# Kernel optimization log

Measured on AMD Instinct MI355X. Metric: run time of the kernel, lower is better.

## Reference

```python
import jax, jax.numpy as jnp
import numpy as np

B, N, D_IN, D_OUT = 8, 2048, 64, 64
ALPHA = 0.2          # LeakyReLU negative slope
MASK_FILL = -9e15    # matches -9000000000000000.0 in the torch code
P_EDGE = 0.05


def _build_adj(key):
    # base random adjacency [N,N], then block structure [[adj, I],[0, adj]]
    base = (jax.random.uniform(key, (N, N)) < P_EDGE).astype(jnp.float32)
    eye = jnp.eye(N, dtype=jnp.float32)
    top = jnp.concatenate([base, eye], axis=1)
    bot = jnp.concatenate([jnp.zeros((N, N), jnp.float32), base], axis=1)
    return jnp.concatenate([top, bot], axis=0)  # [2N, 2N]


def setup_inputs() -> dict:
    key = jax.random.key(0)
    k1, k2, k3, k4, k5, k6 = jax.random.split(key, 6)
    h = jax.random.normal(k1, (B, N, D_IN), jnp.float32)
    ht = jax.random.normal(k2, (B, N, D_IN), jnp.float32)
    # xavier_uniform-ish scale for params
    W = jax.random.normal(k3, (D_IN, D_OUT), jnp.float32) * 0.15
    a1 = jax.random.normal(k4, (D_OUT, 1), jnp.float32) * 0.15
    a2 = jax.random.normal(k5, (D_OUT, 1), jnp.float32) * 0.15
    adj = _build_adj(k6)
    return {"h": h, "ht": ht, "W": W, "a1": a1, "a2": a2, "adj": adj}


def reference(h, ht, W, a1, a2, adj):
    # concat along node dim: [b, 2n, d_in]
    hc = jnp.concatenate([ht, h], axis=1)
    Wh = jnp.einsum('bni,io->bno', hc, W)           # [b, 2n, d_out]
    # additive attention scores: Wh1_i + Wh2_j, LeakyReLU
    Wh1 = Wh @ a1                                    # [b, 2n, 1]
    Wh2 = Wh @ a2                                    # [b, 2n, 1]
    e = Wh1 + jnp.swapaxes(Wh2, 1, 2)                # [b, 2n, 2n]
    e = jnp.where(e > 0, e, ALPHA * e)               # LeakyReLU
    att = jnp.where(adj > 0, e, MASK_FILL)
    att = jax.nn.softmax(att, axis=1)                # NOTE: dim=1 as in torch code
    # dropout is identity in eval mode
    hp = jnp.matmul(att, Wh)                         # [b, 2n, d_out]
    n = adj.shape[0] // 2
    hp = jnp.concatenate([hp[:, :n], hp[:, n:]], axis=-1)  # [b, n, 2*d_out]
    return jax.nn.elu(hp)                            # concat=True -> ELU
```

## Files before the change

### kernel.cpp

```cpp
#include <hip/hip_runtime.h>
#include <hip/hip_bf16.h>
#include <math.h>

#define BB 8
#define NN 2048
#define TN 4096
#define DD 64

typedef __attribute__((ext_vector_type(8))) short short8;
typedef __attribute__((ext_vector_type(4))) float f32x4;
typedef __attribute__((ext_vector_type(4))) unsigned int u32x4;

__device__ __forceinline__ unsigned short f2bf(float f) {
    union { float f; unsigned int i; } v; v.f = f;
    unsigned int r = v.i + 0x7FFF + ((v.i >> 16) & 1);
    return (unsigned short)(r >> 16);
}
__device__ __forceinline__ float bf2f(unsigned short u) {
    union { unsigned int i; float f; } v; v.i = ((unsigned int)u) << 16; return v.f;
}

__global__ __launch_bounds__(256, 4) void k1_wh(
                      const float* __restrict__ h,
                      const float* __restrict__ ht,
                      const float* __restrict__ W,
                      const float* __restrict__ a1,
                      const float* __restrict__ a2,
                      float* __restrict__ Wh,
                      float* __restrict__ E1p, float* __restrict__ E1n,
                      float* __restrict__ E2p, float* __restrict__ E2n,
                      float* __restrict__ E1i) {
    __shared__ float xs[4][512];
    int tid = threadIdx.x;
    int w = tid >> 6, l = tid & 63;
    float wreg[64];
    #pragma unroll
    for (int k = 0; k < 64; ++k) wreg[k] = W[k * 64 + l];
    float a1l = a1[l], a2l = a2[l];
    int rowbase = (blockIdx.x * 4 + w) * 8;
    int b = rowbase >> 12;
    int m0 = rowbase & (TN - 1);
    const float* srcw = (m0 < NN) ? (ht + ((size_t)b * NN + m0) * DD)
                                  : (h  + ((size_t)b * NN + (m0 - NN)) * DD);
    f32x4 g0 = *reinterpret_cast<const f32x4*>(srcw + l * 8);
    f32x4 g1 = *reinterpret_cast<const f32x4*>(srcw + l * 8 + 4);
    *reinterpret_cast<f32x4*>(&xs[w][l * 8])     = g0;
    *reinterpret_cast<f32x4*>(&xs[w][l * 8 + 4]) = g1;
    __syncthreads();
    for (int r = 0; r < 8; ++r) {
        const f32x4* xr = reinterpret_cast<const f32x4*>(&xs[w][r * 64]);
        float c0 = 0.f, c1 = 0.f, c2 = 0.f, c3 = 0.f;
        #pragma unroll
        for (int k = 0; k < 16; ++k) {
            f32x4 s = xr[k];
            c0 += s[0] * wreg[k * 4 + 0];
            c1 += s[1] * wreg[k * 4 + 1];
            c2 += s[2] * wreg[k * 4 + 2];
            c3 += s[3] * wreg[k * 4 + 3];
        }
        float acc = (c0 + c1) + (c2 + c3);
        int m = m0 + r;
        Wh[((size_t)b * TN + m) * DD + l] = acc;
        float r1 = acc * a1l;
        float r2 = acc * a2l;
        #pragma unroll
        for (int off = 32; off > 0; off >>= 1) {
            r1 += __shfl_xor(r1, off, 64);
            r2 += __shfl_xor(r2, off, 64);
        }
        if (l == 0) {
            size_t o = (size_t)b * TN + m;
            float pp = __expf(r1), pn = __expf(0.2f * r1);
            E1p[o] = pp;
            E1n[o] = pn;
            int sp = (b < 4) ? b       : 8 + (b - 4);
            int sn = (b < 4) ? 4 + b   : 12 + (b - 4);
            E1i[(size_t)m * 16 + sp] = pp;
            E1i[(size_t)m * 16 + sn] = pn;
            E2p[o] = __expf(r2);
            E2n[o] = __expf(0.2f * r2);
        }
    }
}

__global__ __launch_bounds__(256) void k2_mask_stats(
    const float* __restrict__ adj,
    const float* __restrict__ E1i,
    const float* __restrict__ E2p, const float* __restrict__ E2n,
    unsigned long long* __restrict__ qmask,
    float* __restrict__ Spart) {
    int tid = threadIdx.x;
    int w = tid >> 6, l = tid & 63;
    int half = blockIdx.z;
    int j = half * 2048 + blockIdx.x * 256 + tid;
    int i0 = half * 2048 + blockIdx.y * 32;
    f32x4 e2p0, e2p1, e2n0, e2n1;
    #pragma unroll
    for (int b = 0; b < 4; ++b) {
        e2p0[b] = E2p[(size_t)b * TN + j];
        e2n0[b] = E2n[(size_t)b * TN + j];
        e2p1[b] = E2p[(size_t)(b + 4) * TN + j];
        e2n1[b] = E2n[(size_t)(b + 4) * TN + j];
    }
    f32x4 acc0 = {0.f, 0.f, 0.f, 0.f}, acc1 = {0.f, 0.f, 0.f, 0.f};
    const f32x4* e1 = reinterpret_cast<const f32x4*>(E1i + (size_t)i0 * 16);
    for (int it8 = 0; it8 < 4; ++it8) {
        float avv[8];
        #pragma unroll
        for (int k = 0; k < 8; ++k)
            avv[k] = adj[(size_t)(i0 + it8 * 8 + k) * TN + j];
        #pragma unroll
        for (int k = 0; k < 8; ++k) {
            int ii = it8 * 8 + k;
            unsigned long long bal = __ballot(avv[k] != 0.f);
            if (l == 0)
                qmask[(size_t)(i0 + ii) * 32 + blockIdx.x * 4 + w] = bal;
            f32x4 P0 = e1[ii * 4 + 0];
            f32x4 N0 = e1[ii * 4 + 1];
            f32x4 P1 = e1[ii * 4 + 2];
            f32x4 N1 = e1[ii * 4 + 3];
            f32x4 v0 = __builtin_elementwise_max(P0 * e2p0, N0 * e2n0);
            f32x4 v1 = __builtin_elementwise_max(P1 * e2p1, N1 * e2n1);
            acc0 += v0 * avv[k];
            acc1 += v1 * avv[k];
        }
    }
    #pragma unroll
    for (int b = 0; b < 4; ++b) {
        Spart[((size_t)blockIdx.y * 8 + b) * TN + j]     = acc0[b];
        Spart[((size_t)blockIdx.y * 8 + b + 4) * TN + j] = acc1[b];
    }
}

__global__ __launch_bounds__(256) void k3_whn(
    const float* __restrict__ Wh,
    const float* __restrict__ Spart,
    const float* __restrict__ E1p, const float* __restrict__ E1n,
    const float* __restrict__ E2p, const float* __restrict__ E2n,
    unsigned short* __restrict__ Wt) {
    __shared__ float tile[64][65];
    __shared__ float ps[4][64];
    __shared__ float rs[64];
    int b = blockIdx.y;
    int j0 = blockIdx.x * 64;
    int tid = threadIdx.x;
    int jj = tid & 63, part = tid >> 6;
    float s = 0.f;
    #pragma unroll
    for (int k = 0; k < 16; ++k) {
        int strip = part * 16 + k;
        s += Spart[((size_t)strip * 8 + b) * TN + j0 + jj];
    }
    ps[part][jj] = s;
    __syncthreads();
    if (tid < 64) {
        float tot = ps[0][tid] + ps[1][tid] + ps[2][tid] + ps[3][tid];
        int j = j0 + tid;
        if (j >= NN) {
            int i = j - NN;
            tot += fmaxf(E1p[(size_t)b * TN + i] * E2p[(size_t)b * TN + j],
                         E1n[(size_t)b * TN + i] * E2n[(size_t)b * TN + j]);
        }
        rs[tid] = 1.0f / tot;
    }
    for (int e = tid; e < 4096; e += 256) {
        int jt = e >> 6, d = e & 63;
        tile[jt][d] = Wh[((size_t)b * TN + j0 + jt) * DD + d];
    }
    __syncthreads();
    for (int e = tid; e < 512; e += 256) {
        int d = e >> 3, jg = e & 7;
        union { unsigned short u[8]; short8 s8; } pk;
        #pragma unroll
        for (int k = 0; k < 8; ++k) {
            int jt = jg * 8 + k;
            pk.u[k] = f2bf(tile[jt][d] * rs[jt]);
        }
        *reinterpret_cast<short8*>(Wt + ((size_t)b * DD + d) * TN + j0 + jg * 8) = pk.s8;
    }
}

__global__ __launch_bounds__(256) void k4_pv(
    const unsigned int* __restrict__ qmask32,
    const float* __restrict__ E1p, const float* __restrict__ E1n,
    const float* __restrict__ E2p, const float* __restrict__ E2n,
    const unsigned short* __restrict__ Wt,
    float* __restrict__ P) {
    __shared__ unsigned short wt_s[64 * 140];
    int bx = blockIdx.x;
    int b  = bx & 7;
    int js = (bx >> 3) & 3;
    int it = bx >> 5;
    int i0 = it * 64;
    int half = (it >= 32);
    int tid = threadIdx.x;
    int w = tid >> 6, l = tid & 63;
    int m = l & 15, q = l >> 4;
    int irow = i0 + w * 16 + m;
    float e1p_v = E1p[(size_t)b * TN + irow];
    float e1n_v = E1n[(size_t)b * TN + irow];
    const float* e2pb = E2p + (size_t)b * TN;
    const float* e2nb = E2n + (size_t)b * TN;
    const unsigned short* wtb = Wt + (size_t)b * DD * TN;
    const unsigned int* mrow = qmask32 + (size_t)irow * 64;

    int r0 = tid >> 4, c0 = tid & 15;
    const int jbase = half * 2048 + js * 512;
    const int jloc0 = js * 512;

    f32x4 acc[4];
    #pragma unroll
    for (int dt = 0; dt < 4; ++dt) acc[dt] = (f32x4){0.f, 0.f, 0.f, 0.f};

    short8 g[4];
    #pragma unroll
    for (int k = 0; k < 4; ++k)
        g[k] = *reinterpret_cast<const short8*>(
            wtb + (size_t)(r0 + 16 * k) * TN + jbase + c0 * 8);

    for (int jt = 0; jt < 4; ++jt) {
        int j0 = jbase + jt * 128;
        __syncthreads();
        #pragma unroll
        for (int k = 0; k < 4; ++k)
            *reinterpret_cast<short8*>(&wt_s[(r0 + 16 * k) * 140 + c0 * 8]) = g[k];
        if (jt < 3) {
            #pragma unroll
            for (int k = 0; k < 4; ++k)
                g[k] = *reinterpret_cast<const short8*>(
                    wtb + (size_t)(r0 + 16 * k) * TN + j0 + 128 + c0 * 8);
        }
        u32x4 m4 = *reinterpret_cast<const u32x4*>(mrow + ((jloc0 + jt * 128) >> 5));
        __syncthreads();

        #pragma unroll
        for (int t = 0; t < 4; ++t) {
            int jb = j0 + t * 32 + q * 8;
            unsigned int bytev = (m4[t] >> (q * 8)) & 0xFFu;
            f32x4 p20 = *reinterpret_cast<const f32x4*>(e2pb + jb);
            f32x4 p21 = *reinterpret_cast<const f32x4*>(e2pb + jb + 4);
            f32x4 n20 = *reinterpret_cast<const f32x4*>(e2nb + jb);
            f32x4 n21 = *reinterpret_cast<const f32x4*>(e2nb + jb + 4);
            f32x4 v0 = __builtin_elementwise_max(p20 * e1p_v, n20 * e1n_v);
            f32x4 v1 = __builtin_elementwise_max(p21 * e1p_v, n21 * e1n_v);
            union { f32x4 f; u32x4 u; } uv0, uv1;
            uv0.f = v0; uv1.f = v1;
            u32x4 mk0, mk1;
            #pragma unroll
            for (int c = 0; c < 4; ++c) {
                mk0[c] = (unsigned int)((int)(bytev << (31 - c)) >> 31);
                mk1[c] = (unsigned int)((int)(bytev << (27 - c)) >> 31);
            }
            uv0.u &= mk0; uv1.u &= mk1;
            union { unsigned int u[4]; short8 s8; } af;
            __hip_bfloat162 hb0 = __float22bfloat162_rn(make_float2(uv0.f[0], uv0.f[1]));
            __hip_bfloat162 hb1 = __float22bfloat162_rn(make_float2(uv0.f[2], uv0.f[3]));
            __hip_bfloat162 hb2 = __float22bfloat162_rn(make_float2(uv1.f[0], uv1.f[1]));
            __hip_bfloat162 hb3 = __float22bfloat162_rn(make_float2(uv1.f[2], uv1.f[3]));
            af.u[0] = *reinterpret_cast<unsigned int*>(&hb0);
            af.u[1] = *reinterpret_cast<unsigned int*>(&hb1);
            af.u[2] = *reinterpret_cast<unsigned int*>(&hb2);
            af.u[3] = *reinterpret_cast<unsigned int*>(&hb3);
            #pragma unroll
            for (int dt = 0; dt < 4; ++dt) {
                short8 bf = *reinterpret_cast<const short8*>(
                    &wt_s[(dt * 16 + m) * 140 + t * 32 + q * 8]);
                acc[dt] = __builtin_amdgcn_mfma_f32_16x16x32_bf16(af.s8, bf, acc[dt], 0, 0, 0);
            }
        }
    }

    int gbase = i0 + w * 16 + q * 4;
    if (half == 0 && js == 0) {
        #pragma unroll
        for (int r = 0; r < 4; ++r) {
            int gg = gbase + r;
            float ed = fmaxf(E1p[(size_t)b * TN + gg] * e2pb[gg + NN],
                             E1n[(size_t)b * TN + gg] * e2nb[gg + NN]);
            #pragma unroll
            for (int dt = 0; dt < 4; ++dt) {
                int d = dt * 16 + m;
                acc[dt][r] += ed * bf2f(wtb[(size_t)d * TN + gg + NN]);
            }
        }
    }

    float* Pb = P + ((size_t)(js * 8 + b)) * TN * DD;
    #pragma unroll
    for (int r = 0; r < 4; ++r) {
        size_t rowoff = (size_t)(gbase + r) * DD + m;
        #pragma unroll
        for (int dt = 0; dt < 4; ++dt)
            Pb[rowoff + dt * 16] = acc[dt][r];
    }
}

__global__ void k5_epi(const float* __restrict__ P,
                       float* __restrict__ out) {
    int t = blockIdx.x * 256 + threadIdx.x;
    int d4 = t & 31;
    int n = (t >> 5) & 2047;
    int b = t >> 16;
    int i = (d4 < 16) ? n : (n + NN);
    int d = (d4 < 16) ? (d4 * 4) : ((d4 - 16) * 4);
    f32x4 s = {0.f, 0.f, 0.f, 0.f};
    #pragma unroll
    for (int js = 0; js < 4; ++js)
        s += *reinterpret_cast<const f32x4*>(
            P + (((size_t)(js * 8 + b)) * TN + i) * DD + d);
    f32x4 rr;
    #pragma unroll
    for (int c = 0; c < 4; ++c) rr[c] = (s[c] > 0.f) ? s[c] : expm1f(s[c]);
    *reinterpret_cast<f32x4*>(out + ((size_t)b * NN + n) * 128 + d4 * 4) = rr;
}

extern "C" void kernel_launch(void* const* d_in, const int* in_sizes, int n_in,
                              void* d_out, int out_size, void* d_ws, size_t ws_size,
                              hipStream_t stream) {
    const float* h   = (const float*)d_in[0];
    const float* ht  = (const float*)d_in[1];
    const float* W   = (const float*)d_in[2];
    const float* a1  = (const float*)d_in[3];
    const float* a2  = (const float*)d_in[4];
    const float* adj = (const float*)d_in[5];
    float* out = (float*)d_out;

    char* ws = (char*)d_ws;
    float* Wh          = (float*)(ws);
    float* Spart       = (float*)(ws + (8 << 20));
    unsigned short* Wt = (unsigned short*)(ws + (16 << 20));
    float* E1p         = (float*)(ws + (20 << 20));
    float* E1n         = (float*)(ws + (20 << 20) + (128 << 10));
    float* E2p         = (float*)(ws + (20 << 20) + (256 << 10));
    float* E2n         = (float*)(ws + (20 << 20) + (384 << 10));
    unsigned long long* qmask = (unsigned long long*)(ws + (20 << 20) + (512 << 10));
    float* E1i         = (float*)(ws + (20 << 20) + (512 << 10) + (2 << 20));
    const unsigned int* qmask32 = (const unsigned int*)qmask;
    float* P           = (float*)(ws + (24 << 20));

    k1_wh<<<dim3(BB * TN / 32), dim3(256), 0, stream>>>(h, ht, W, a1, a2, Wh,
                                                        E1p, E1n, E2p, E2n, E1i);
    k2_mask_stats<<<dim3(8, 64, 2), dim3(256), 0, stream>>>(adj, E1i, E2p, E2n,
                                                            qmask, Spart);
    k3_whn<<<dim3(64, 8), dim3(256), 0, stream>>>(Wh, Spart, E1p, E1n, E2p, E2n, Wt);
    k4_pv<<<dim3(2048), dim3(256), 0, stream>>>(qmask32, E1p, E1n, E2p, E2n, Wt, P);
    k5_epi<<<dim3(2048), dim3(256), 0, stream>>>(P, out);
}
```

Measured before the change: 172.1 us.

## Restructure PV kernel to single-wave blocks reading Wt directly, batch k1 reductions

k4 now runs one 64-thread wave per block covering 32 rows (two 16-row MFMA tiles) and reads B fragments straight from global/L2 instead of staging them through LDS with block barriers. Each Wt fragment is reused for two row tiles, which raises reuse per load and removes the syncthreads. In k1, the per-row 64-lane shuffle reductions for the attention dot products are replaced by one LDS transpose and a 3-step shuffle over 8 rows at once. The risks are uncoalesced strided global reads of Wt in k4 and lower occupancy per CU.

```diff
diff --git a/kernel.cpp b/kernel.cpp
--- a/kernel.cpp
+++ b/kernel.cpp
@@ -31,12 +31,14 @@
                       float* __restrict__ E2p, float* __restrict__ E2n,
                       float* __restrict__ E1i) {
     __shared__ float xs[4][512];
+    __shared__ float tr[4][8 * 68];
+    __shared__ float ab[128];
     int tid = threadIdx.x;
     int w = tid >> 6, l = tid & 63;
     float wreg[64];
     #pragma unroll
     for (int k = 0; k < 64; ++k) wreg[k] = W[k * 64 + l];
-    float a1l = a1[l], a2l = a2[l];
+    if (tid < 128) ab[tid] = (tid < 64) ? a1[tid] : a2[tid - 64];
     int rowbase = (blockIdx.x * 4 + w) * 8;
     int b = rowbase >> 12;
     int m0 = rowbase & (TN - 1);
@@ -47,6 +49,8 @@
     *reinterpret_cast<f32x4*>(&xs[w][l * 8])     = g0;
     *reinterpret_cast<f32x4*>(&xs[w][l * 8 + 4]) = g1;
     __syncthreads();
+    float acc8[8];
+    #pragma unroll
     for (int r = 0; r < 8; ++r) {
         const f32x4* xr = reinterpret_cast<const f32x4*>(&xs[w][r * 64]);
         float c0 = 0.f, c1 = 0.f, c2 = 0.f, c3 = 0.f;
@@ -58,28 +62,39 @@
             c2 += s[2] * wreg[k * 4 + 2];
             c3 += s[3] * wreg[k * 4 + 3];
         }
-        float acc = (c0 + c1) + (c2 + c3);
-        int m = m0 + r;
-        Wh[((size_t)b * TN + m) * DD + l] = acc;
-        float r1 = acc * a1l;
-        float r2 = acc * a2l;
-        #pragma unroll
-        for (int off = 32; off > 0; off >>= 1) {
-            r1 += __shfl_xor(r1, off, 64);
-            r2 += __shfl_xor(r2, off, 64);
-        }
-        if (l == 0) {
-            size_t o = (size_t)b * TN + m;
-            float pp = __expf(r1), pn = __expf(0.2f * r1);
-            E1p[o] = pp;
-            E1n[o] = pn;
-            int sp = (b < 4) ? b       : 8 + (b - 4);
-            int sn = (b < 4) ? 4 + b   : 12 + (b - 4);
-            E1i[(size_t)m * 16 + sp] = pp;
-            E1i[(size_t)m * 16 + sn] = pn;
-            E2p[o] = __expf(r2);
-            E2n[o] = __expf(0.2f * r2);
-        }
+        acc8[r] = (c0 + c1) + (c2 + c3);
+        Wh[((size_t)b * TN + m0 + r) * DD + l] = acc8[r];
+    }
+    #pragma unroll
+    for (int r = 0; r < 8; ++r) tr[w][r * 68 + l] = acc8[r];
+    int rr = l >> 3, cc = l & 7;
+    f32x4 va  = *reinterpret_cast<const f32x4*>(&tr[w][rr * 68 + cc * 8]);
+    f32x4 vb  = *reinterpret_cast<const f32x4*>(&tr[w][rr * 68 + cc * 8 + 4]);
+    f32x4 a1a = *reinterpret_cast<const f32x4*>(&ab[cc * 8]);
+    f32x4 a1b = *reinterpret_cast<const f32x4*>(&ab[cc * 8 + 4]);
+    f32x4 a2a = *reinterpret_cast<const f32x4*>(&ab[64 + cc * 8]);
+    f32x4 a2b = *reinterpret_cast<const f32x4*>(&ab[64 + cc * 8 + 4]);
+    f32x4 s1v = va * a1a + vb * a1b;
+    f32x4 s2v = va * a2a + vb * a2b;
+    float p1 = (s1v[0] + s1v[1]) + (s1v[2] + s1v[3]);
+    float p2 = (s2v[0] + s2v[1]) + (s2v[2] + s2v[3]);
+    #pragma unroll
+    for (int off = 1; off <= 4; off <<= 1) {
+        p1 += __shfl_xor(p1, off, 64);
+        p2 += __shfl_xor(p2, off, 64);
+    }
+    if (cc == 0) {
+        int mrow = m0 + rr;
+        size_t o = (size_t)b * TN + mrow;
+        float pp = __expf(p1), pn = __expf(0.2f * p1);
+        E1p[o] = pp;
+        E1n[o] = pn;
+        int sp = (b < 4) ? b       : 8 + (b - 4);
+        int sn = (b < 4) ? 4 + b   : 12 + (b - 4);
+        E1i[(size_t)mrow * 16 + sp] = pp;
+        E1i[(size_t)mrow * 16 + sn] = pn;
+        E2p[o] = __expf(p2);
+        E2n[o] = __expf(0.2f * p2);
     }
 }
 
@@ -180,118 +195,110 @@
     }
 }
 
-__global__ __launch_bounds__(256) void k4_pv(
+#define K4_BUILD_AF(af_, by_, e1p_, e1n_)                                     \
+    {                                                                         \
+        f32x4 v0 = __builtin_elementwise_max(p2a * e1p_, n2a * e1n_);         \
+        f32x4 v1 = __builtin_elementwise_max(p2b * e1p_, n2b * e1n_);         \
+        union { f32x4 f; u32x4 u; } uv0, uv1;                                 \
+        uv0.f = v0; uv1.f = v1;                                               \
+        u32x4 mk0, mk1;                                                       \
+        _Pragma("unroll")                                                     \
+        for (int c = 0; c < 4; ++c) {                                         \
+            mk0[c] = (unsigned int)((int)(by_ << (31 - c)) >> 31);            \
+            mk1[c] = (unsigned int)((int)(by_ << (27 - c)) >> 31);            \
+        }                                                                     \
+        uv0.u &= mk0; uv1.u &= mk1;                                           \
+        __hip_bfloat162 hb0 = __float22bfloat162_rn(make_float2(uv0.f[0], uv0.f[1])); \
+        __hip_bfloat162 hb1 = __float22bfloat162_rn(make_float2(uv0.f[2], uv0.f[3])); \
+        __hip_bfloat162 hb2 = __float22bfloat162_rn(make_float2(uv1.f[0], uv1.f[1])); \
+        __hip_bfloat162 hb3 = __float22bfloat162_rn(make_float2(uv1.f[2], uv1.f[3])); \
+        af_.u[0] = *reinterpret_cast<unsigned int*>(&hb0);                    \
+        af_.u[1] = *reinterpret_cast<unsigned int*>(&hb1);                    \
+        af_.u[2] = *reinterpret_cast<unsigned int*>(&hb2);                    \
+        af_.u[3] = *reinterpret_cast<unsigned int*>(&hb3);                    \
+    }
+
+__global__ __launch_bounds__(64, 3) void k4_pv(
     const unsigned int* __restrict__ qmask32,
     const float* __restrict__ E1p, const float* __restrict__ E1n,
     const float* __restrict__ E2p, const float* __restrict__ E2n,
     const unsigned short* __restrict__ Wt,
     float* __restrict__ P) {
-    __shared__ unsigned short wt_s[64 * 140];
     int bx = blockIdx.x;
     int b  = bx & 7;
     int js = (bx >> 3) & 3;
     int it = bx >> 5;
-    int i0 = it * 64;
-    int half = (it >= 32);
-    int tid = threadIdx.x;
-    int w = tid >> 6, l = tid & 63;
+    int i0 = it * 32;
+    int half = (it >= 64);
+    int l = threadIdx.x;
     int m = l & 15, q = l >> 4;
-    int irow = i0 + w * 16 + m;
-    float e1p_v = E1p[(size_t)b * TN + irow];
-    float e1n_v = E1n[(size_t)b * TN + irow];
     const float* e2pb = E2p + (size_t)b * TN;
     const float* e2nb = E2n + (size_t)b * TN;
     const unsigned short* wtb = Wt + (size_t)b * DD * TN;
-    const unsigned int* mrow = qmask32 + (size_t)irow * 64;
-
-    int r0 = tid >> 4, c0 = tid & 15;
+    int ir0 = i0 + m, ir1 = i0 + 16 + m;
+    float e1p0 = E1p[(size_t)b * TN + ir0], e1n0 = E1n[(size_t)b * TN + ir0];
+    float e1p1 = E1p[(size_t)b * TN + ir1], e1n1 = E1n[(size_t)b * TN + ir1];
+    const unsigned int* mr0 = qmask32 + (size_t)ir0 * 64 + js * 16;
+    const unsigned int* mr1 = qmask32 + (size_t)ir1 * 64 + js * 16;
     const int jbase = half * 2048 + js * 512;
-    const int jloc0 = js * 512;
-
-    f32x4 acc[4];
-    #pragma unroll
-    for (int dt = 0; dt < 4; ++dt) acc[dt] = (f32x4){0.f, 0.f, 0.f, 0.f};
-
-    short8 g[4];
-    #pragma unroll
-    for (int k = 0; k < 4; ++k)
-        g[k] = *reinterpret_cast<const short8*>(
-            wtb + (size_t)(r0 + 16 * k) * TN + jbase + c0 * 8);
-
-    for (int jt = 0; jt < 4; ++jt) {
-        int j0 = jbase + jt * 128;
-        __syncthreads();
-        #pragma unroll
-        for (int k = 0; k < 4; ++k)
-            *reinterpret_cast<short8*>(&wt_s[(r0 + 16 * k) * 140 + c0 * 8]) = g[k];
-        if (jt < 3) {
-            #pragma unroll
-            for (int k = 0; k < 4; ++k)
-                g[k] = *reinterpret_cast<const short8*>(
-                    wtb + (size_t)(r0 + 16 * k) * TN + j0 + 128 + c0 * 8);
-        }
-        u32x4 m4 = *reinterpret_cast<const u32x4*>(mrow + ((jloc0 + jt * 128) >> 5));
-        __syncthreads();
-
+
+    f32x4 acc0[4], acc1[4];
+    #pragma unroll
+    for (int dt = 0; dt < 4; ++dt) {
+        acc0[dt] = (f32x4){0.f, 0.f, 0.f, 0.f};
+        acc1[dt] = (f32x4){0.f, 0.f, 0.f, 0.f};
+    }
+
+    for (int kb = 0; kb < 4; ++kb) {
+        u32x4 m40 = *reinterpret_cast<const u32x4*>(mr0 + kb * 4);
+        u32x4 m41 = *reinterpret_cast<const u32x4*>(mr1 + kb * 4);
         #pragma unroll
         for (int t = 0; t < 4; ++t) {
-            int jb = j0 + t * 32 + q * 8;
-            unsigned int bytev = (m4[t] >> (q * 8)) & 0xFFu;
-            f32x4 p20 = *reinterpret_cast<const f32x4*>(e2pb + jb);
-            f32x4 p21 = *reinterpret_cast<const f32x4*>(e2pb + jb + 4);
-            f32x4 n20 = *reinterpret_cast<const f32x4*>(e2nb + jb);
-            f32x4 n21 = *reinterpret_cast<const f32x4*>(e2nb + jb + 4);
-            f32x4 v0 = __builtin_elementwise_max(p20 * e1p_v, n20 * e1n_v);
-            f32x4 v1 = __builtin_elementwise_max(p21 * e1p_v, n21 * e1n_v);
-            union { f32x4 f; u32x4 u; } uv0, uv1;
-            uv0.f = v0; uv1.f = v1;
-            u32x4 mk0, mk1;
-            #pragma unroll
-            for (int c = 0; c < 4; ++c) {
-                mk0[c] = (unsigned int)((int)(bytev << (31 - c)) >> 31);
-                mk1[c] = (unsigned int)((int)(bytev << (27 - c)) >> 31);
-            }
-            uv0.u &= mk0; uv1.u &= mk1;
-            union { unsigned int u[4]; short8 s8; } af;
-            __hip_bfloat162 hb0 = __float22bfloat162_rn(make_float2(uv0.f[0], uv0.f[1]));
-            __hip_bfloat162 hb1 = __float22bfloat162_rn(make_float2(uv0.f[2], uv0.f[3]));
-            __hip_bfloat162 hb2 = __float22bfloat162_rn(make_float2(uv1.f[0], uv1.f[1]));
-            __hip_bfloat162 hb3 = __float22bfloat162_rn(make_float2(uv1.f[2], uv1.f[3]));
-            af.u[0] = *reinterpret_cast<unsigned int*>(&hb0);
-            af.u[1] = *reinterpret_cast<unsigned int*>(&hb1);
-            af.u[2] = *reinterpret_cast<unsigned int*>(&hb2);
-            af.u[3] = *reinterpret_cast<unsigned int*>(&hb3);
+            int jb = jbase + kb * 128 + t * 32 + q * 8;
+            f32x4 p2a = *reinterpret_cast<const f32x4*>(e2pb + jb);
+            f32x4 p2b = *reinterpret_cast<const f32x4*>(e2pb + jb + 4);
+            f32x4 n2a = *reinterpret_cast<const f32x4*>(e2nb + jb);
+            f32x4 n2b = *reinterpret_cast<const f32x4*>(e2nb + jb + 4);
+            unsigned int by0 = (m40[t] >> (q * 8)) & 0xFFu;
+            unsigned int by1 = (m41[t] >> (q * 8)) & 0xFFu;
+            union { unsigned int u[4]; short8 s8; } af0, af1;
+            K4_BUILD_AF(af0, by0, e1p0, e1n0)
+            K4_BUILD_AF(af1, by1, e1p1, e1n1)
             #pragma unroll
             for (int dt = 0; dt < 4; ++dt) {
                 short8 bf = *reinterpret_cast<const short8*>(
-                    &wt_s[(dt * 16 + m) * 140 + t * 32 + q * 8]);
-                acc[dt] = __builtin_amdgcn_mfma_f32_16x16x32_bf16(af.s8, bf, acc[dt], 0, 0, 0);
+                    wtb + (size_t)(dt * 16 + m) * TN + jb);
+                acc0[dt] = __builtin_amdgcn_mfma_f32_16x16x32_bf16(af0.s8, bf, acc0[dt], 0, 0, 0);
+                acc1[dt] = __builtin_amdgcn_mfma_f32_16x16x32_bf16(af1.s8, bf, acc1[dt], 0, 0, 0);
             }
         }
     }
 
-    int gbase = i0 + w * 16 + q * 4;
-    if (half == 0 && js == 0) {
+    float* Pb = P + ((size_t)(js * 8 + b)) * TN * DD;
+    #pragma unroll
+    for (int g = 0; g < 2; ++g) {
+        int gbase = i0 + g * 16 + q * 4;
         #pragma unroll
         for (int r = 0; r < 4; ++r) {
             int gg = gbase + r;
-            float ed = fmaxf(E1p[(size_t)b * TN + gg] * e2pb[gg + NN],
-                             E1n[(size_t)b * TN + gg] * e2nb[gg + NN]);
-            #pragma unroll
-            for (int dt = 0; dt < 4; ++dt) {
-                int d = dt * 16 + m;
-                acc[dt][r] += ed * bf2f(wtb[(size_t)d * TN + gg + NN]);
+            float a0 = (g == 0) ? acc0[0][r] : acc1[0][r];
+            float a1_ = (g == 0) ? acc0[1][r] : acc1[1][r];
+            float a2_ = (g == 0) ? acc0[2][r] : acc1[2][r];
+            float a3 = (g == 0) ? acc0[3][r] : acc1[3][r];
+            if (half == 0 && js == 0) {
+                float ed = fmaxf(E1p[(size_t)b * TN + gg] * e2pb[gg + NN],
+                                 E1n[(size_t)b * TN + gg] * e2nb[gg + NN]);
+                a0 += ed * bf2f(wtb[(size_t)(0 * 16 + m) * TN + gg + NN]);
+                a1_ += ed * bf2f(wtb[(size_t)(1 * 16 + m) * TN + gg + NN]);
+                a2_ += ed * bf2f(wtb[(size_t)(2 * 16 + m) * TN + gg + NN]);
+                a3 += ed * bf2f(wtb[(size_t)(3 * 16 + m) * TN + gg + NN]);
             }
-        }
-    }
-
-    float* Pb = P + ((size_t)(js * 8 + b)) * TN * DD;
-    #pragma unroll
-    for (int r = 0; r < 4; ++r) {
-        size_t rowoff = (size_t)(gbase + r) * DD + m;
-        #pragma unroll
-        for (int dt = 0; dt < 4; ++dt)
-            Pb[rowoff + dt * 16] = acc[dt][r];
+            size_t rowoff = (size_t)gg * DD + m;
+            Pb[rowoff + 0]  = a0;
+            Pb[rowoff + 16] = a1_;
+            Pb[rowoff + 32] = a2_;
+            Pb[rowoff + 48] = a3;
+        }
     }
 }
 
@@ -343,6 +350,6 @@
     k2_mask_stats<<<dim3(8, 64, 2), dim3(256), 0, stream>>>(adj, E1i, E2p, E2n,
                                                             qmask, Spart);
     k3_whn<<<dim3(64, 8), dim3(256), 0, stream>>>(Wh, Spart, E1p, E1n, E2p, E2n, Wt);
-    k4_pv<<<dim3(2048), dim3(256), 0, stream>>>(qmask32, E1p, E1n, E2p, E2n, Wt, P);
+    k4_pv<<<dim3(4096), dim3(64), 0, stream>>>(qmask32, E1p, E1n, E2p, E2n, Wt, P);
     k5_epi<<<dim3(2048), dim3(256), 0, stream>>>(P, out);
 }
```

Measured after the change: 185.6 us. +7.8%, slower.
